# Kernel tuning notes

Measured on AMD Instinct MI355X. Metric: run time of the kernel, lower is better.

Reference implementation:

```python
import jax, jax.numpy as jnp
import numpy as np

B, S, D, H = 4, 2048, 1024, 16
HD = D // H  # head dim = 64


def setup_inputs() -> dict:
    key = jax.random.key(0)
    ks = jax.random.split(key, 8)
    s = 1.0 / np.sqrt(D)
    return {
        "query": jax.random.normal(ks[0], (B, S, D), jnp.float32),
        "key": jax.random.normal(ks[1], (B, S, D), jnp.float32),
        "value": jax.random.normal(ks[2], (B, S, D), jnp.float32),
        "wq": jax.random.normal(ks[3], (D, D), jnp.float32) * s,
        "wk": jax.random.normal(ks[4], (D, D), jnp.float32) * s,
        "wv": jax.random.normal(ks[5], (D, D), jnp.float32) * s,
        "wo": jax.random.normal(ks[6], (D, D), jnp.float32) * s,
        "bo": jax.random.normal(ks[7], (D,), jnp.float32) * s,
    }


def reference(query, key, value, wq, wk, wv, wo, bo):
    # project and split heads: [B,S,D] -> [B,H,S,HD]
    def split_heads(x, w):
        return (x @ w.T).reshape(B, S, H, HD).transpose(0, 2, 1, 3)

    q = split_heads(query, wq)
    k = split_heads(key, wk)
    v = split_heads(value, wv)
    scores = jnp.einsum('bhqd,bhkd->bhqk', q, k) / jnp.sqrt(jnp.float32(HD))
    attn = jax.nn.softmax(scores, axis=-1)
    out = jnp.einsum('bhqk,bhkd->bhqd', attn, v)
    out = out.transpose(0, 2, 1, 3).reshape(B, S, D)
    return out @ wo.T + bo
```

## Files before the change

### kernel.cpp

```cpp
#include <hip/hip_runtime.h>
#include <stdint.h>


#define NSEQ 2048
#define NDIM 1024
#define NE   8388608

typedef unsigned short u16;
typedef unsigned int   u32;
typedef __bf16 bf16x8 __attribute__((ext_vector_type(8)));
typedef float  f32x4  __attribute__((ext_vector_type(4)));

__device__ __forceinline__ u16 f2bf(float f) {
  return (u16)((__builtin_bit_cast(u32, f) + 0x8000u) >> 16);
}
__device__ __forceinline__ u32 pack_bf2(float lo, float hi) {
  u32 a = __builtin_bit_cast(u32, lo) + 0x8000u;
  u32 b = __builtin_bit_cast(u32, hi) + 0x8000u;
  return __builtin_amdgcn_perm(b, a, 0x07060302);
}

__device__ __forceinline__ void async_load16(const u16* gsrc, u16* ldst) {
  __builtin_amdgcn_global_load_lds(
      (const __attribute__((address_space(1))) void*)gsrc,
      (__attribute__((address_space(3))) void*)ldst, 16, 0, 0);
}

__device__ __forceinline__ void conv_body(const float* __restrict__ src,
                                          u16* __restrict__ dst, int blk) {
  const int i = blk * 256 + (int)threadIdx.x;
  const float4 a = ((const float4*)src)[2 * i];
  const float4 b = ((const float4*)src)[2 * i + 1];
  uint4 o;
  o.x = pack_bf2(a.x, a.y); o.y = pack_bf2(a.z, a.w);
  o.z = pack_bf2(b.x, b.y); o.w = pack_bf2(b.z, b.w);
  ((uint4*)dst)[i] = o;
}
__global__ __launch_bounds__(256) void conv_big_kernel(
    const float* __restrict__ query, const float* __restrict__ keyi,
    const float* __restrict__ value, u16* __restrict__ Xq,
    u16* __restrict__ Xk, u16* __restrict__ Xv) {
  int blk = blockIdx.x;
  const float* src; u16* dst;
  if (blk < 4096)      { src = query; dst = Xq; }
  else if (blk < 8192) { src = keyi;  dst = Xk; blk -= 4096; }
  else                 { src = value; dst = Xv; blk -= 8192; }
  conv_body(src, dst, blk);
}
__global__ __launch_bounds__(256) void conv_w_kernel(
    const float* __restrict__ wq, const float* __restrict__ wk,
    const float* __restrict__ wv, const float* __restrict__ wo,
    u16* __restrict__ Wall) {
  int blk = blockIdx.x;
  const int z = blk >> 9;
  blk &= 511;
  const float* src = (z == 0) ? wq : (z == 1) ? wk : (z == 2) ? wv : wo;
  conv_body(src, Wall + (size_t)z * 1048576, blk);
}

template <bool OUTF32, bool BIAS>
__device__ __forceinline__ void gemm_core(const u16* __restrict__ A,
                                          const u16* __restrict__ B,
                                          void* __restrict__ Yv,
                                          const float* __restrict__ bias,
                                          float scale, long m0, long n0,
                                          long ldy) {
  __shared__ u16 At[128 * 32];
  __shared__ u16 Bt[128 * 32];
  const int t    = threadIdx.x;
  const int lane = t & 63;
  const int w    = t >> 6;
  const int m    = lane & 15;
  const int q    = lane >> 4;
  const int wr   = w >> 1;
  const int wc   = w & 1;
  const int srow = t >> 2;
  const int scol = (t & 3) * 8;

  f32x4 acc[4][4];
#pragma unroll
  for (int i = 0; i < 4; i++)
#pragma unroll
    for (int j = 0; j < 4; j++) acc[i][j] = (f32x4){0.f, 0.f, 0.f, 0.f};

  for (int k0 = 0; k0 < NDIM; k0 += 32) {
    __syncthreads();
    async_load16(A + (m0 + srow) * NDIM + k0 + scol, At + w * 512);
    async_load16(A + (m0 + 64 + srow) * NDIM + k0 + scol, At + 2048 + w * 512);
    async_load16(B + (n0 + srow) * NDIM + k0 + scol, Bt + w * 512);
    async_load16(B + (n0 + 64 + srow) * NDIM + k0 + scol, Bt + 2048 + w * 512);
    __syncthreads();

    bf16x8 a[4], b[4];
#pragma unroll
    for (int mi = 0; mi < 4; mi++)
      a[mi] = *(const bf16x8*)(At + (wr * 64 + mi * 16 + m) * 32 + q * 8);
#pragma unroll
    for (int ni = 0; ni < 4; ni++)
      b[ni] = *(const bf16x8*)(Bt + (wc * 64 + ni * 16 + m) * 32 + q * 8);
#pragma unroll
    for (int mi = 0; mi < 4; mi++)
#pragma unroll
      for (int ni = 0; ni < 4; ni++)
        acc[mi][ni] = __builtin_amdgcn_mfma_f32_16x16x32_bf16(a[mi], b[ni], acc[mi][ni], 0, 0, 0);
  }

#pragma unroll
  for (int mi = 0; mi < 4; mi++) {
#pragma unroll
    for (int ni = 0; ni < 4; ni++) {
      const long row0 = m0 + wr * 64 + mi * 16 + q * 4;
      const long col  = n0 + wc * 64 + ni * 16 + m;
      float badd = 0.f;
      if (BIAS) badd = bias[col];
#pragma unroll
      for (int r = 0; r < 4; r++) {
        const float v = acc[mi][ni][r] * scale + badd;
        if (OUTF32) ((float*)Yv)[(row0 + r) * ldy + col] = v;
        else        ((u16*)Yv)[(row0 + r) * ldy + col] = f2bf(v);
      }
    }
  }
}

__global__ __launch_bounds__(256) void gemm_qkv_kernel(
    const u16* __restrict__ Xq, const u16* __restrict__ Xk,
    const u16* __restrict__ Xv, const u16* __restrict__ Wall,
    u16* __restrict__ Qp, u16* __restrict__ Kp, u16* __restrict__ Vt) {
  const int z = blockIdx.z;
  if (z < 2) {
    const u16* A = z ? Xk : Xq;
    const u16* B = Wall + (size_t)z * 1048576;
    u16* Y       = z ? Kp : Qp;
    gemm_core<false, false>(A, B, Y, nullptr, z ? 1.0f : 0.18033688f,
                            (long)blockIdx.x * 128, (long)blockIdx.y * 128, NDIM);
  } else {
    const int flat = blockIdx.y * 64 + blockIdx.x;
    const long b   = flat >> 7;
    const int rem  = flat & 127;
    gemm_core<false, false>(Wall + 2 * 1048576, Xv + b * NSEQ * NDIM,
                            Vt + b * (long)NDIM * NSEQ, nullptr, 1.0f,
                            (long)(rem >> 4) * 128, (long)(rem & 15) * 128, NSEQ);
  }
}

__global__ __launch_bounds__(256) void gemm_out_kernel(
    const u16* __restrict__ A, const u16* __restrict__ Wall,
    float* __restrict__ Y, const float* __restrict__ bias) {
  gemm_core<true, true>(A, Wall + 3 * 1048576, Y, bias, 1.0f,
                        (long)blockIdx.x * 128, (long)blockIdx.y * 128, NDIM);
}

__global__ __launch_bounds__(256, 4) void attn_kernel(
    const u16* __restrict__ Qp, const u16* __restrict__ Kp,
    const u16* __restrict__ Vtg, u16* __restrict__ Op) {
  __shared__ u16 Kt[64 * 72];
  __shared__ u16 Vt[64 * 72];
  const int t    = threadIdx.x;
  const int lane = t & 63;
  const int w    = t >> 6;
  const int m    = lane & 15;
  const int q    = lane >> 4;
  const int bh   = blockIdx.y;
  const int b    = bh >> 4;
  const int h    = bh & 15;
  const int wq0  = blockIdx.x * 128 + w * 32;
  const long base_bh = (long)b * NSEQ * NDIM + h * 64;
  const long vbase   = (long)b * NDIM * NSEQ + (long)(h * 64) * NSEQ;

  bf16x8 qf[2][2];
#pragma unroll
  for (int qi = 0; qi < 2; qi++)
#pragma unroll
    for (int ks = 0; ks < 2; ks++)
      qf[qi][ks] = *(const bf16x8*)(Qp + base_bh + (long)(wq0 + qi * 16 + m) * NDIM + ks * 32 + q * 8);

  f32x4 ot[2][4];
#pragma unroll
  for (int qi = 0; qi < 2; qi++)
#pragma unroll
    for (int mb = 0; mb < 4; mb++) ot[qi][mb] = (f32x4){0.f, 0.f, 0.f, 0.f};
  float lp[2] = {0.f, 0.f};

  const int srow = t >> 3;
  const int c8   = t & 7;
  const int scol = c8 * 8;

  const int vnb   = c8 >> 1;
  const int vbase_c = 32 * (vnb >> 1) + 4 * (vnb & 1);
  const int vcol0 = vbase_c + 8 * ((2 * c8) & 3);
  const int vcol1 = vbase_c + 8 * ((2 * c8 + 1) & 3);

  const u16* kgp = Kp + base_bh + (long)srow * NDIM + scol;
  const u16* vgp = Vtg + vbase + (long)srow * NSEQ + scol;

  int4 kr0 = *(const int4*)(kgp);
  int4 kr1 = *(const int4*)(kgp + 32l * NDIM);
  int4 vr0 = *(const int4*)(vgp);
  int4 vr1 = *(const int4*)(vgp + 32l * NSEQ);

  const f32x4 zz = (f32x4){0.f, 0.f, 0.f, 0.f};

  for (int kt = 0; kt < NSEQ / 64; kt++) {
    __syncthreads();
    *(int4*)(Kt + srow * 72 + scol)        = kr0;
    *(int4*)(Kt + (srow + 32) * 72 + scol) = kr1;
    *(uint2*)(Vt + srow * 72 + vcol0)        = make_uint2((u32)vr0.x, (u32)vr0.y);
    *(uint2*)(Vt + srow * 72 + vcol1)        = make_uint2((u32)vr0.z, (u32)vr0.w);
    *(uint2*)(Vt + (srow + 32) * 72 + vcol0) = make_uint2((u32)vr1.x, (u32)vr1.y);
    *(uint2*)(Vt + (srow + 32) * 72 + vcol1) = make_uint2((u32)vr1.z, (u32)vr1.w);
    __syncthreads();

    if (kt < NSEQ / 64 - 1) {
      const long k1 = (long)(kt + 1) * 64;
      kr0 = *(const int4*)(kgp + k1 * NDIM);
      kr1 = *(const int4*)(kgp + (k1 + 32) * NDIM);
      vr0 = *(const int4*)(vgp + k1);
      vr1 = *(const int4*)(vgp + 32l * NSEQ + k1);
    }

    f32x4 st[2][4];
    __builtin_amdgcn_s_setprio(1);
#pragma unroll
    for (int nb = 0; nb < 4; nb++) {
      bf16x8 kf = *(const bf16x8*)(Kt + (nb * 16 + m) * 72 + q * 8);
      st[0][nb] = __builtin_amdgcn_mfma_f32_16x16x32_bf16(kf, qf[0][0], zz, 0, 0, 0);
      st[1][nb] = __builtin_amdgcn_mfma_f32_16x16x32_bf16(kf, qf[1][0], zz, 0, 0, 0);
    }
#pragma unroll
    for (int nb = 0; nb < 4; nb++) {
      bf16x8 kf = *(const bf16x8*)(Kt + (nb * 16 + m) * 72 + 32 + q * 8);
      st[0][nb] = __builtin_amdgcn_mfma_f32_16x16x32_bf16(kf, qf[0][1], st[0][nb], 0, 0, 0);
      st[1][nb] = __builtin_amdgcn_mfma_f32_16x16x32_bf16(kf, qf[1][1], st[1][nb], 0, 0, 0);
    }
    __builtin_amdgcn_s_setprio(0);

    u32 pkx[2][4], pky[2][4];
#pragma unroll
    for (int qi = 0; qi < 2; qi++)
#pragma unroll
      for (int nb = 0; nb < 4; nb++) {
        const float p0 = __builtin_amdgcn_exp2f(st[qi][nb][0]);
        const float p1 = __builtin_amdgcn_exp2f(st[qi][nb][1]);
        const float p2 = __builtin_amdgcn_exp2f(st[qi][nb][2]);
        const float p3 = __builtin_amdgcn_exp2f(st[qi][nb][3]);
        lp[qi] += (p0 + p1) + (p2 + p3);
        pkx[qi][nb] = pack_bf2(p0, p1);
        pky[qi][nb] = pack_bf2(p2, p3);
      }

    __builtin_amdgcn_s_setprio(1);
#pragma unroll
    for (int ks2 = 0; ks2 < 2; ks2++) {
      bf16x8 pf[2];
#pragma unroll
      for (int qi = 0; qi < 2; qi++) {
        uint4 pw;
        pw.x = pkx[qi][2 * ks2];
        pw.y = pky[qi][2 * ks2];
        pw.z = pkx[qi][2 * ks2 + 1];
        pw.w = pky[qi][2 * ks2 + 1];
        pf[qi] = __builtin_bit_cast(bf16x8, pw);
      }
#pragma unroll
      for (int mb = 0; mb < 4; mb++) {
        bf16x8 vf = *(const bf16x8*)(Vt + (mb * 16 + m) * 72 + ks2 * 32 + q * 8);
        ot[0][mb] = __builtin_amdgcn_mfma_f32_16x16x32_bf16(vf, pf[0], ot[0][mb], 0, 0, 0);
        ot[1][mb] = __builtin_amdgcn_mfma_f32_16x16x32_bf16(vf, pf[1], ot[1][mb], 0, 0, 0);
      }
    }
    __builtin_amdgcn_s_setprio(0);
  }

  float rinv[2];
#pragma unroll
  for (int qi = 0; qi < 2; qi++) {
    float v = lp[qi];
    v += __shfl_xor(v, 16);
    v += __shfl_xor(v, 32);
    rinv[qi] = 1.0f / v;
  }

  __syncthreads();
  u16* ept = Kt + w * 1152;
#pragma unroll
  for (int qi = 0; qi < 2; qi++) {
#pragma unroll
    for (int mb = 0; mb < 4; mb++) {
      uint2 pk;
      pk.x = pack_bf2(ot[qi][mb][0] * rinv[qi], ot[qi][mb][1] * rinv[qi]);
      pk.y = pack_bf2(ot[qi][mb][2] * rinv[qi], ot[qi][mb][3] * rinv[qi]);
      *(uint2*)(ept + m * 72 + mb * 16 + q * 4) = pk;
    }
#pragma unroll
    for (int c = 0; c < 2; c++) {
      const int u   = c * 64 + lane;
      const int qr  = u >> 3;
      const int oct = u & 7;
      const int4 val = *(const int4*)(ept + qr * 72 + oct * 8);
      const long s   = wq0 + qi * 16 + qr;
      *(int4*)(Op + base_bh + s * NDIM + oct * 8) = val;
    }
  }
}

extern "C" void kernel_launch(void* const* d_in, const int* in_sizes, int n_in,
                              void* d_out, int out_size, void* d_ws, size_t ws_size,
                              hipStream_t stream) {
  const float* query = (const float*)d_in[0];
  const float* keyi  = (const float*)d_in[1];
  const float* value = (const float*)d_in[2];
  const float* wq    = (const float*)d_in[3];
  const float* wk    = (const float*)d_in[4];
  const float* wv    = (const float*)d_in[5];
  const float* wo    = (const float*)d_in[6];
  const float* bo    = (const float*)d_in[7];

  u16* ws = (u16*)d_ws;
  u16* Qp = ws;
  u16* Kp = ws + (size_t)NE;
  u16* Vt = ws + 2 * (size_t)NE;
  u16* XqO = ws + 3 * (size_t)NE;

  u16* Xk = (u16*)d_out;
  u16* Xv = (u16*)d_out + (size_t)NE;
  u16* Wall = (u16*)d_in[0];

  dim3 blk(256, 1, 1);
  conv_big_kernel<<<dim3(12288, 1, 1), blk, 0, stream>>>(query, keyi, value, XqO, Xk, Xv);
  conv_w_kernel<<<dim3(2048, 1, 1), blk, 0, stream>>>(wq, wk, wv, wo, Wall);
  gemm_qkv_kernel<<<dim3(64, 8, 3), blk, 0, stream>>>(XqO, Xk, Xv, Wall, Qp, Kp, Vt);
  attn_kernel<<<dim3(16, 64, 1), blk, 0, stream>>>(Qp, Kp, Vt, XqO);
  gemm_out_kernel<<<dim3(64, 8, 1), blk, 0, stream>>>(XqO, Wall, (float*)d_out, bo);
}
```

Before: 337.2 us.

## Double-buffer attention K/V LDS tiles and compute row sums with MFMA

The attention kernel now uses two LDS buffers for K and V tiles. Staging the next tile overlaps with compute on the current one, which cuts the barriers per tile from two to one. The softmax denominator is now accumulated by an extra MFMA against a ones vector instead of scalar adds and cross-lane shuffles, and bf16 packing uses the hardware v_cvt_pk_bf16_f32 instruction. Doubling LDS per block may lower occupancy, and the extra MFMAs add matrix-core work. The kernel appears to skip max subtraction, so there is no online max to track.

New measurement: 349.4 us. +3.6%, slower.

```diff
diff --git a/kernel.cpp b/kernel.cpp
--- a/kernel.cpp
+++ b/kernel.cpp
@@ -18,6 +18,11 @@
   u32 a = __builtin_bit_cast(u32, lo) + 0x8000u;
   u32 b = __builtin_bit_cast(u32, hi) + 0x8000u;
   return __builtin_amdgcn_perm(b, a, 0x07060302);
+}
+__device__ __forceinline__ u32 cvt_pk_bf16(float lo, float hi) {
+  u32 r;
+  asm("v_cvt_pk_bf16_f32 %0, %1, %2" : "=v"(r) : "v"(lo), "v"(hi));
+  return r;
 }
 
 __device__ __forceinline__ void async_load16(const u16* gsrc, u16* ldst) {
@@ -154,8 +159,8 @@
 __global__ __launch_bounds__(256, 4) void attn_kernel(
     const u16* __restrict__ Qp, const u16* __restrict__ Kp,
     const u16* __restrict__ Vtg, u16* __restrict__ Op) {
-  __shared__ u16 Kt[64 * 72];
-  __shared__ u16 Vt[64 * 72];
+  __shared__ u16 Kt[2][64 * 72];
+  __shared__ u16 Vt[2][64 * 72];
   const int t    = threadIdx.x;
   const int lane = t & 63;
   const int w    = t >> 6;
@@ -175,12 +180,16 @@
     for (int ks = 0; ks < 2; ks++)
       qf[qi][ks] = *(const bf16x8*)(Qp + base_bh + (long)(wq0 + qi * 16 + m) * NDIM + ks * 32 + q * 8);
 
+  const f32x4 zz = (f32x4){0.f, 0.f, 0.f, 0.f};
   f32x4 ot[2][4];
 #pragma unroll
   for (int qi = 0; qi < 2; qi++)
 #pragma unroll
-    for (int mb = 0; mb < 4; mb++) ot[qi][mb] = (f32x4){0.f, 0.f, 0.f, 0.f};
-  float lp[2] = {0.f, 0.f};
+    for (int mb = 0; mb < 4; mb++) ot[qi][mb] = zz;
+  f32x4 lsum[2] = {zz, zz};
+  uint4 onesw;
+  onesw.x = onesw.y = onesw.z = onesw.w = 0x3F803F80u;
+  const bf16x8 onesf = __builtin_bit_cast(bf16x8, onesw);
 
   const int srow = t >> 3;
   const int c8   = t & 7;
@@ -194,42 +203,27 @@
   const u16* kgp = Kp + base_bh + (long)srow * NDIM + scol;
   const u16* vgp = Vtg + vbase + (long)srow * NSEQ + scol;
 
-  int4 kr0 = *(const int4*)(kgp);
-  int4 kr1 = *(const int4*)(kgp + 32l * NDIM);
-  int4 vr0 = *(const int4*)(vgp);
-  int4 vr1 = *(const int4*)(vgp + 32l * NSEQ);
-
-  const f32x4 zz = (f32x4){0.f, 0.f, 0.f, 0.f};
-
-  for (int kt = 0; kt < NSEQ / 64; kt++) {
-    __syncthreads();
-    *(int4*)(Kt + srow * 72 + scol)        = kr0;
-    *(int4*)(Kt + (srow + 32) * 72 + scol) = kr1;
-    *(uint2*)(Vt + srow * 72 + vcol0)        = make_uint2((u32)vr0.x, (u32)vr0.y);
-    *(uint2*)(Vt + srow * 72 + vcol1)        = make_uint2((u32)vr0.z, (u32)vr0.w);
-    *(uint2*)(Vt + (srow + 32) * 72 + vcol0) = make_uint2((u32)vr1.x, (u32)vr1.y);
-    *(uint2*)(Vt + (srow + 32) * 72 + vcol1) = make_uint2((u32)vr1.z, (u32)vr1.w);
-    __syncthreads();
-
-    if (kt < NSEQ / 64 - 1) {
-      const long k1 = (long)(kt + 1) * 64;
-      kr0 = *(const int4*)(kgp + k1 * NDIM);
-      kr1 = *(const int4*)(kgp + (k1 + 32) * NDIM);
-      vr0 = *(const int4*)(vgp + k1);
-      vr1 = *(const int4*)(vgp + 32l * NSEQ + k1);
-    }
-
+  auto stage = [&](int bi, int4 k0, int4 k1, int4 v0, int4 v1) {
+    *(int4*)(Kt[bi] + srow * 72 + scol)        = k0;
+    *(int4*)(Kt[bi] + (srow + 32) * 72 + scol) = k1;
+    *(uint2*)(Vt[bi] + srow * 72 + vcol0)        = make_uint2((u32)v0.x, (u32)v0.y);
+    *(uint2*)(Vt[bi] + srow * 72 + vcol1)        = make_uint2((u32)v0.z, (u32)v0.w);
+    *(uint2*)(Vt[bi] + (srow + 32) * 72 + vcol0) = make_uint2((u32)v1.x, (u32)v1.y);
+    *(uint2*)(Vt[bi] + (srow + 32) * 72 + vcol1) = make_uint2((u32)v1.z, (u32)v1.w);
+  };
+
+  auto compute = [&](const u16* KT, const u16* VT) {
     f32x4 st[2][4];
     __builtin_amdgcn_s_setprio(1);
 #pragma unroll
     for (int nb = 0; nb < 4; nb++) {
-      bf16x8 kf = *(const bf16x8*)(Kt + (nb * 16 + m) * 72 + q * 8);
+      bf16x8 kf = *(const bf16x8*)(KT + (nb * 16 + m) * 72 + q * 8);
       st[0][nb] = __builtin_amdgcn_mfma_f32_16x16x32_bf16(kf, qf[0][0], zz, 0, 0, 0);
       st[1][nb] = __builtin_amdgcn_mfma_f32_16x16x32_bf16(kf, qf[1][0], zz, 0, 0, 0);
     }
 #pragma unroll
     for (int nb = 0; nb < 4; nb++) {
-      bf16x8 kf = *(const bf16x8*)(Kt + (nb * 16 + m) * 72 + 32 + q * 8);
+      bf16x8 kf = *(const bf16x8*)(KT + (nb * 16 + m) * 72 + 32 + q * 8);
       st[0][nb] = __builtin_amdgcn_mfma_f32_16x16x32_bf16(kf, qf[0][1], st[0][nb], 0, 0, 0);
       st[1][nb] = __builtin_amdgcn_mfma_f32_16x16x32_bf16(kf, qf[1][1], st[1][nb], 0, 0, 0);
     }
@@ -244,9 +238,8 @@
         const float p1 = __builtin_amdgcn_exp2f(st[qi][nb][1]);
         const float p2 = __builtin_amdgcn_exp2f(st[qi][nb][2]);
         const float p3 = __builtin_amdgcn_exp2f(st[qi][nb][3]);
-        lp[qi] += (p0 + p1) + (p2 + p3);
-        pkx[qi][nb] = pack_bf2(p0, p1);
-        pky[qi][nb] = pack_bf2(p2, p3);
+        pkx[qi][nb] = cvt_pk_bf16(p0, p1);
+        pky[qi][nb] = cvt_pk_bf16(p2, p3);
       }
 
     __builtin_amdgcn_s_setprio(1);
@@ -264,32 +257,63 @@
       }
 #pragma unroll
       for (int mb = 0; mb < 4; mb++) {
-        bf16x8 vf = *(const bf16x8*)(Vt + (mb * 16 + m) * 72 + ks2 * 32 + q * 8);
+        bf16x8 vf = *(const bf16x8*)(VT + (mb * 16 + m) * 72 + ks2 * 32 + q * 8);
         ot[0][mb] = __builtin_amdgcn_mfma_f32_16x16x32_bf16(vf, pf[0], ot[0][mb], 0, 0, 0);
         ot[1][mb] = __builtin_amdgcn_mfma_f32_16x16x32_bf16(vf, pf[1], ot[1][mb], 0, 0, 0);
       }
+      lsum[0] = __builtin_amdgcn_mfma_f32_16x16x32_bf16(onesf, pf[0], lsum[0], 0, 0, 0);
+      lsum[1] = __builtin_amdgcn_mfma_f32_16x16x32_bf16(onesf, pf[1], lsum[1], 0, 0, 0);
     }
     __builtin_amdgcn_s_setprio(0);
+  };
+
+  int4 ka0 = *(const int4*)(kgp);
+  int4 ka1 = *(const int4*)(kgp + 32l * NDIM);
+  int4 va0 = *(const int4*)(vgp);
+  int4 va1 = *(const int4*)(vgp + 32l * NSEQ);
+  stage(0, ka0, ka1, va0, va1);
+  int4 kb0 = *(const int4*)(kgp + 64l * NDIM);
+  int4 kb1 = *(const int4*)(kgp + 96l * NDIM);
+  int4 vb0 = *(const int4*)(vgp + 64);
+  int4 vb1 = *(const int4*)(vgp + 32l * NSEQ + 64);
+  __syncthreads();
+
+  for (int kt = 0; kt < NSEQ / 64; kt += 2) {
+    if (kt + 2 < NSEQ / 64) {
+      const long o = (long)(kt + 2) * 64;
+      ka0 = *(const int4*)(kgp + o * NDIM);
+      ka1 = *(const int4*)(kgp + (o + 32) * NDIM);
+      va0 = *(const int4*)(vgp + o);
+      va1 = *(const int4*)(vgp + 32l * NSEQ + o);
+    }
+    stage(1, kb0, kb1, vb0, vb1);
+    compute(Kt[0], Vt[0]);
+    __syncthreads();
+
+    if (kt + 3 < NSEQ / 64) {
+      const long o = (long)(kt + 3) * 64;
+      kb0 = *(const int4*)(kgp + o * NDIM);
+      kb1 = *(const int4*)(kgp + (o + 32) * NDIM);
+      vb0 = *(const int4*)(vgp + o);
+      vb1 = *(const int4*)(vgp + 32l * NSEQ + o);
+    }
+    if (kt + 2 < NSEQ / 64) stage(0, ka0, ka1, va0, va1);
+    compute(Kt[1], Vt[1]);
+    __syncthreads();
   }
 
   float rinv[2];
 #pragma unroll
-  for (int qi = 0; qi < 2; qi++) {
-    float v = lp[qi];
-    v += __shfl_xor(v, 16);
-    v += __shfl_xor(v, 32);
-    rinv[qi] = 1.0f / v;
-  }
-
-  __syncthreads();
-  u16* ept = Kt + w * 1152;
+  for (int qi = 0; qi < 2; qi++) rinv[qi] = 1.0f / lsum[qi][0];
+
+  u16* ept = Kt[0] + w * 1152;
 #pragma unroll
   for (int qi = 0; qi < 2; qi++) {
 #pragma unroll
     for (int mb = 0; mb < 4; mb++) {
       uint2 pk;
-      pk.x = pack_bf2(ot[qi][mb][0] * rinv[qi], ot[qi][mb][1] * rinv[qi]);
-      pk.y = pack_bf2(ot[qi][mb][2] * rinv[qi], ot[qi][mb][3] * rinv[qi]);
+      pk.x = cvt_pk_bf16(ot[qi][mb][0] * rinv[qi], ot[qi][mb][1] * rinv[qi]);
+      pk.y = cvt_pk_bf16(ot[qi][mb][2] * rinv[qi], ot[qi][mb][3] * rinv[qi]);
       *(uint2*)(ept + m * 72 + mb * 16 + q * 4) = pk;
     }
 #pragma unroll
```
